# Kernel tuning notes

Hardware: AMD Instinct MI355X
Metric: run time of the kernel (lower is better)

The kernel has to match this reference:

```python
import jax, jax.numpy as jnp
import numpy as np

B, S, D = 1, 2048, 2048
HQ, HKV = 32, 8
HD = D // HQ            # 64
G = HQ // HKV           # 4 query heads per kv head


def setup_inputs() -> dict:
    key = jax.random.key(0)
    ks = jax.random.split(key, 5)
    x = jax.random.normal(ks[0], (B, S, D), jnp.float32)
    # RoPE tables (theta = 10000), shape [S, HD//2]
    inv_freq = 1.0 / (10000.0 ** (np.arange(0, HD, 2, dtype=np.float64) / HD))
    angles = np.outer(np.arange(S, dtype=np.float64), inv_freq)
    freqs_cos = jnp.asarray(np.cos(angles), jnp.float32)
    freqs_sin = jnp.asarray(np.sin(angles), jnp.float32)
    # additive causal mask [1,1,S,S]: 0 on/below diagonal, large negative above
    i = jnp.arange(S)
    causal_mask = jnp.where(i[None, :] <= i[:, None], 0.0, -1e9).astype(jnp.float32)[None, None]
    sc = 1.0 / np.sqrt(D)
    Wq = jax.random.normal(ks[1], (D, HQ * HD), jnp.float32) * sc
    Wk = jax.random.normal(ks[2], (D, HKV * HD), jnp.float32) * sc
    Wv = jax.random.normal(ks[3], (D, HKV * HD), jnp.float32) * sc
    Wo = jax.random.normal(ks[4], (D, D), jnp.float32) * sc
    return {"x": x, "freqs_cos": freqs_cos, "freqs_sin": freqs_sin,
            "causal_mask": causal_mask, "Wq": Wq, "Wk": Wk, "Wv": Wv, "Wo": Wo}


def _rope(t, cos, sin):
    # t: [B,S,H,HD]; complex multiply on interleaved (even, odd) pairs
    b, s, h, d = t.shape
    t2 = t.reshape(b, s, h, d // 2, 2)
    t0, t1 = t2[..., 0], t2[..., 1]
    c = cos[None, :, None, :]
    sn = sin[None, :, None, :]
    out = jnp.stack([t0 * c - t1 * sn, t0 * sn + t1 * c], axis=-1)
    return out.reshape(b, s, h, d)


def reference(x, freqs_cos, freqs_sin, causal_mask, Wq, Wk, Wv, Wo):
    b, s, _ = x.shape
    q = (x @ Wq).reshape(b, s, HQ, HD)
    k = (x @ Wk).reshape(b, s, HKV, HD)
    v = (x @ Wv).reshape(b, s, HKV, HD)
    q = _rope(q, freqs_cos, freqs_sin)
    k = _rope(k, freqs_cos, freqs_sin)
    # GQA without materializing repeat_kv: group query heads per kv head
    q = q.transpose(0, 2, 1, 3).reshape(b, HKV, G, s, HD)   # [b,kv,g,s,d]
    k = k.transpose(0, 2, 1, 3)                              # [b,kv,s,d]
    v = v.transpose(0, 2, 1, 3)                              # [b,kv,s,d]
    scores = jnp.einsum('bkgsd,bktd->bkgst', q, k) / jnp.sqrt(jnp.float32(HD))
    scores = scores + causal_mask[:, :, None]                # [1,1,1,S,S] broadcast
    probs = jax.nn.softmax(scores, axis=-1)
    out = jnp.einsum('bkgst,bktd->bkgsd', probs, v)          # [b,kv,g,s,d]
    out = out.transpose(0, 3, 1, 2, 4).reshape(b, s, D)      # merge heads in (kv,g) order
    return out @ Wo
```

## Files before the change

### kernel.cpp

```cpp
#include <hip/hip_runtime.h>

#define SEQ 2048
#define DMODEL 2048

typedef __attribute__((ext_vector_type(8))) _Float16 half8;
typedef __attribute__((ext_vector_type(4))) float f32x4;
typedef __attribute__((ext_vector_type(16))) float f32x16;

typedef const __attribute__((address_space(1))) void* gptr_t;
typedef __attribute__((address_space(3))) void* lptr_t;

static __device__ __forceinline__ void gload16(const void* g, void* l) {
  __builtin_amdgcn_global_load_lds((gptr_t)g, (lptr_t)l, 16, 0, 0);
}

static __device__ __forceinline__ unsigned short f2h(float f) {
  _Float16 h = (_Float16)f;
  union { _Float16 h; unsigned short u; } v; v.h = h;
  return v.u;
}

static __device__ __forceinline__ unsigned int pkh2(float a, float b) {
  union { __fp16 __attribute__((ext_vector_type(2))) h; unsigned int u; } v;
  v.h = __builtin_amdgcn_cvt_pkrtz(a, b);
  return v.u;
}

__global__ void k_cvt(const float* __restrict__ in, unsigned short* __restrict__ out, int n) {
  int i = (blockIdx.x * 256 + threadIdx.x) * 4;
  if (i >= n) return;
  float4 v = *(const float4*)(in + i);
  ushort4 o;
  o.x = f2h(v.x); o.y = f2h(v.y); o.z = f2h(v.z); o.w = f2h(v.w);
  *(ushort4*)(out + i) = o;
}

__global__ void k_tcvt(const float* __restrict__ in, unsigned short* __restrict__ out,
                       int K, int N, int ldin) {
  __shared__ float tile[32][33];
  int n0 = blockIdx.x * 32, k0 = blockIdx.y * 32;
  int tx = threadIdx.x, ty = threadIdx.y;
  #pragma unroll
  for (int j = ty; j < 32; j += 8)
    tile[j][tx] = in[(long)(k0 + j) * ldin + n0 + tx];
  __syncthreads();
  #pragma unroll
  for (int j = ty; j < 32; j += 8)
    out[(long)(n0 + j) * K + k0 + tx] = f2h(tile[tx][j]);
}

__global__ void k_tvp(const unsigned short* __restrict__ in, unsigned short* __restrict__ out) {
  __shared__ unsigned short tile[32][33];
  int c0 = blockIdx.x * 32, s0 = blockIdx.y * 32;
  int tx = threadIdx.x, ty = threadIdx.y;
  #pragma unroll
  for (int j = ty; j < 32; j += 8)
    tile[j][tx] = in[(long)(s0 + j) * 512 + c0 + tx];
  __syncthreads();
  #pragma unroll
  for (int j = ty; j < 32; j += 8) {
    int c = c0 + j;
    int s = s0 + tx;
    int sp = (s & ~12) | ((s & 8) >> 1) | ((s & 4) << 1);
    out[((long)(c >> 6) * 64 + (c & 63)) * SEQ + sp] = tile[tx][j];
  }
}

static __device__ __forceinline__ bool gemm_core(const unsigned short* __restrict__ A,
                                                 const unsigned short* __restrict__ B,
                                                 int K, char* SM, long m0, long n0,
                                                 int& wmO, int& wnO, f32x4 acc[4][4]) {
  int t = threadIdx.x;
  int l = t & 63, w = t >> 6;
  int ks = w & 1, wm = (w >> 2) & 1, wn = (w >> 1) & 1;
  int lr = l & 15, lh = l >> 4;
  wmO = wm; wnO = wn;
  unsigned short* As = (unsigned short*)SM;
  unsigned short* Bs = (unsigned short*)(SM + 32768);

  const unsigned short* Ag = A + (m0 + (t >> 3)) * K + (((t & 7) ^ ((t >> 3) & 7)) * 8);
  const unsigned short* Bg = B + (n0 + (t >> 3)) * K + (((t & 7) ^ ((t >> 3) & 7)) * 8);

  #pragma unroll
  for (int i = 0; i < 4; i++)
    #pragma unroll
    for (int j = 0; j < 4; j++)
      acc[i][j] = (f32x4){0.f, 0.f, 0.f, 0.f};

#define STG(buf, k0) do { \
    gload16(Ag + (k0), As + (buf) * 8192 + t * 8); \
    gload16(Ag + 64 * K + (k0), As + (buf) * 8192 + 4096 + t * 8); \
    gload16(Bg + (k0), Bs + (buf) * 8192 + t * 8); \
    gload16(Bg + 64 * K + (k0), Bs + (buf) * 8192 + 4096 + t * 8); \
  } while (0)

  int T = K >> 6;
  STG(0, 0);
  asm volatile("s_waitcnt vmcnt(0)" ::: "memory");
  __builtin_amdgcn_s_barrier();

  for (int ph = 0; ph < T; ph++) {
    if (ph + 1 < T) STG((ph + 1) & 1, (ph + 1) * 64);
    const unsigned short* Ab = As + (ph & 1) * 8192;
    const unsigned short* Bb = Bs + (ph & 1) * 8192;
    half8 a[4], b[4];
    #pragma unroll
    for (int mf = 0; mf < 4; mf++) {
      int ra = wm * 64 + mf * 16 + lr;
      a[mf] = *(const half8*)&Ab[ra * 64 + (((ks * 4 + lh) ^ (ra & 7)) * 8)];
    }
    #pragma unroll
    for (int nf = 0; nf < 4; nf++) {
      int rb = wn * 64 + nf * 16 + lr;
      b[nf] = *(const half8*)&Bb[rb * 64 + (((ks * 4 + lh) ^ (rb & 7)) * 8)];
    }
    #pragma unroll
    for (int mf = 0; mf < 4; mf++)
      #pragma unroll
      for (int nf = 0; nf < 4; nf++)
        acc[mf][nf] = __builtin_amdgcn_mfma_f32_16x16x32_f16(a[mf], b[nf], acc[mf][nf], 0, 0, 0);
    asm volatile("s_waitcnt vmcnt(0)" ::: "memory");
    __builtin_amdgcn_s_barrier();
  }
#undef STG

  __syncthreads();
  float* red = (float*)SM;
  int p = wm * 2 + wn;
  if (ks == 1) {
    #pragma unroll
    for (int mf = 0; mf < 4; mf++)
      #pragma unroll
      for (int nf = 0; nf < 4; nf++)
        *(f32x4*)&red[p * 4096 + l * 64 + (((mf * 4 + nf) ^ (l & 15)) << 2)] = acc[mf][nf];
  }
  __syncthreads();
  if (ks == 0) {
    #pragma unroll
    for (int mf = 0; mf < 4; mf++)
      #pragma unroll
      for (int nf = 0; nf < 4; nf++)
        acc[mf][nf] += *(const f32x4*)&red[p * 4096 + l * 64 + (((mf * 4 + nf) ^ (l & 15)) << 2)];
  }
  return ks == 0;
}

__global__ __launch_bounds__(512) void k_gemm(const unsigned short* __restrict__ A,
                                              const unsigned short* __restrict__ B,
                                              float* __restrict__ C, int M, int N, int K) {
  __shared__ __align__(16) char SM[65536];
  int l = threadIdx.x & 63;
  int lr = l & 15, lh = l >> 4;
  long m0 = (long)blockIdx.y * 128, n0 = (long)blockIdx.x * 128;
  f32x4 acc[4][4];
  int wm, wn;
  bool own = gemm_core(A, B, K, SM, m0, n0, wm, wn, acc);
  if (own) {
    #pragma unroll
    for (int mf = 0; mf < 4; mf++)
      #pragma unroll
      for (int nf = 0; nf < 4; nf++)
        #pragma unroll
        for (int i = 0; i < 4; i++)
          C[(m0 + wm * 64 + mf * 16 + lh * 4 + i) * N + n0 + wn * 64 + nf * 16 + lr] = acc[mf][nf][i];
  }
}

__global__ __launch_bounds__(512) void k_gemm_qkv(const unsigned short* __restrict__ A,
                                                  const unsigned short* __restrict__ B,
                                                  unsigned short* __restrict__ Qr,
                                                  unsigned short* __restrict__ Kr,
                                                  unsigned short* __restrict__ Vr,
                                                  const float* __restrict__ fc,
                                                  const float* __restrict__ fs, int K) {
  __shared__ __align__(16) char SM[65536];
  int l = threadIdx.x & 63;
  int lr = l & 15, lh = l >> 4;
  long m0 = (long)blockIdx.y * 128, n0 = (long)blockIdx.x * 128;
  f32x4 acc[4][4];
  int wm, wn;
  bool own = gemm_core(A, B, K, SM, m0, n0, wm, wn, acc);
  if (!own) return;

  const float SC = 0.125f * 1.44269504f;
  int n0i = (int)n0;
  if (n0i < 2560) {
    bool isQ = n0i < 2048;
    float scl = isQ ? SC : 1.0f;
    #pragma unroll
    for (int mf = 0; mf < 4; mf++)
      #pragma unroll
      for (int i = 0; i < 4; i++) {
        int row = (int)m0 + wm * 64 + mf * 16 + lh * 4 + i;
        const float* fcr = fc + row * 32;
        const float* fsr = fs + row * 32;
        #pragma unroll
        for (int nf = 0; nf < 4; nf++) {
          float v = acc[mf][nf][i];
          float pv = __shfl_xor(v, 1);
          int col = n0i + wn * 64 + nf * 16 + lr;
          int j = (col & 63) >> 1;
          float c_ = fcr[j] * scl, s_ = fsr[j] * scl;
          float o = (lr & 1) ? (pv * s_ + v * c_) : (v * c_ - pv * s_);
          if (isQ) Qr[(long)row * 2048 + col] = f2h(o);
          else {
            int cc = col - 2048;
            Kr[((long)(cc >> 6) * SEQ + row) * 64 + (cc & 63)] = f2h(o);
          }
        }
      }
  } else {
    #pragma unroll
    for (int mf = 0; mf < 4; mf++)
      #pragma unroll
      for (int i = 0; i < 4; i++) {
        int row = (int)m0 + wm * 64 + mf * 16 + lh * 4 + i;
        #pragma unroll
        for (int nf = 0; nf < 4; nf++) {
          int col = n0i + wn * 64 + nf * 16 + lr;
          Vr[(long)row * 512 + (col - 2560)] = f2h(acc[mf][nf][i]);
        }
      }
  }
}

template <bool DG>
static __device__ __forceinline__ void attn_tile(const unsigned short* __restrict__ Ks,
                                                 const unsigned short* __restrict__ Vs,
                                                 int q, int hs, const half8 (&Qf)[4],
                                                 f32x16& O0, f32x16& O1, float& lsum) {
  half8 Kf[4], Vf[2][2];
  #pragma unroll
  for (int d = 0; d < 4; d++) {
    int e0 = d * 16 + 8 * hs;
    Kf[d] = *(const half8*)&Ks[q * 64 + (e0 ^ ((q & 7) << 3))];
  }
  #pragma unroll
  for (int ks = 0; ks < 2; ks++)
    #pragma unroll
    for (int nf = 0; nf < 2; nf++)
      Vf[ks][nf] = *(const half8*)&Vs[(2 * ks + hs) * 512 + (q + 32 * nf) * 8];

  f32x16 S;
  #pragma unroll
  for (int r = 0; r < 16; r++) S[r] = 0.f;
  #pragma unroll
  for (int d = 0; d < 4; d++)
    S = __builtin_amdgcn_mfma_f32_32x32x16_f16(Kf[d], Qf[d], S, 0, 0, 0);

  float p[16];
  #pragma unroll
  for (int r = 0; r < 16; r++) {
    float v = S[r];
    if (DG) {
      int key = (r & 3) + 8 * (r >> 2) + 4 * hs;
      if (key > q) v = -1e30f;
    }
    p[r] = __builtin_exp2f(v - 8.0f);
    lsum += p[r];
  }

  union { unsigned int u[4]; half8 hh; } f0, f1;
  #pragma unroll
  for (int c = 0; c < 4; c++) {
    f0.u[c] = pkh2(p[2 * c], p[2 * c + 1]);
    f1.u[c] = pkh2(p[8 + 2 * c], p[9 + 2 * c]);
  }

  O0 = __builtin_amdgcn_mfma_f32_32x32x16_f16(f0.hh, Vf[0][0], O0, 0, 0, 0);
  O0 = __builtin_amdgcn_mfma_f32_32x32x16_f16(f1.hh, Vf[1][0], O0, 0, 0, 0);
  O1 = __builtin_amdgcn_mfma_f32_32x32x16_f16(f0.hh, Vf[0][1], O1, 0, 0, 0);
  O1 = __builtin_amdgcn_mfma_f32_32x32x16_f16(f1.hh, Vf[1][1], O1, 0, 0, 0);
}

__global__ __launch_bounds__(256) void k_attn(const unsigned short* __restrict__ Qr,
                                              const unsigned short* __restrict__ Kr,
                                              const unsigned short* __restrict__ Vg,
                                              unsigned short* __restrict__ AO) {
  __shared__ unsigned short KT[2][8192];
  __shared__ unsigned short VT[2][8192];
  __shared__ float gbuf[4][32];

  int tt = threadIdx.x;
  int wid = tt >> 6, l = tt & 63;
  int q = l & 31, hs = l >> 5;
  int h = blockIdx.x, hkv = h >> 2;
  int by = (int)gridDim.y - 1 - blockIdx.y;
  int dt = 4 * by + wid;
  int q0 = by * 128 + wid * 32;

  const unsigned short* Kh = Kr + (long)hkv * SEQ * 64;
  const unsigned short* Vh = Vg + (long)hkv * 64 * SEQ;

  int skr = tt >> 3, skc = tt & 7;
  const unsigned short* Ksrc = Kh + (long)skr * 64 + ((skc * 8) ^ ((skr & 7) << 3));
  const unsigned short* Vsrc = Vh + (long)(tt & 63) * SEQ + ((tt >> 6) * 8);

#define ASTAGE(si) do { \
    int buf_ = (si) & 1; \
    _Pragma("unroll") for (int sub_ = 0; sub_ < 4; sub_++) { \
      int t0_ = ((si) * 4 + sub_) * 32; \
      gload16(Ksrc + (long)t0_ * 64, &KT[buf_][sub_ * 2048 + tt * 8]); \
      gload16(Vsrc + t0_, &VT[buf_][sub_ * 2048 + tt * 8]); \
    } \
  } while (0)

  half8 Qf[4];
  #pragma unroll
  for (int d = 0; d < 4; d++)
    Qf[d] = *(const half8*)&Qr[(long)(q0 + q) * 2048 + h * 64 + d * 16 + 8 * hs];

  f32x16 O0, O1;
  #pragma unroll
  for (int r = 0; r < 16; r++) { O0[r] = 0.f; O1[r] = 0.f; }
  float lsum = 0.f;

  ASTAGE(0);
  asm volatile("s_waitcnt vmcnt(0)" ::: "memory");
  __builtin_amdgcn_s_barrier();

  for (int si = 0; si <= by; si++) {
    if (si + 1 <= by) ASTAGE(si + 1);

    int buf = si & 1;
    const unsigned short* Kb = &KT[buf][0];
    const unsigned short* Vb = &VT[buf][0];
    int rem = dt - si * 4 + 1;
    if (rem > 4) {
      attn_tile<false>(Kb, Vb, q, hs, Qf, O0, O1, lsum);
      attn_tile<false>(Kb + 2048, Vb + 2048, q, hs, Qf, O0, O1, lsum);
      attn_tile<false>(Kb + 4096, Vb + 4096, q, hs, Qf, O0, O1, lsum);
      attn_tile<false>(Kb + 6144, Vb + 6144, q, hs, Qf, O0, O1, lsum);
    } else if (rem > 0) {
      for (int sub = 0; sub < rem - 1; sub++)
        attn_tile<false>(Kb + sub * 2048, Vb + sub * 2048, q, hs, Qf, O0, O1, lsum);
      attn_tile<true>(Kb + (rem - 1) * 2048, Vb + (rem - 1) * 2048, q, hs, Qf, O0, O1, lsum);
    }

    asm volatile("s_waitcnt vmcnt(0)" ::: "memory");
    __builtin_amdgcn_s_barrier();
  }
#undef ASTAGE

  lsum += __shfl_xor(lsum, 32);
  if (l < 32) gbuf[wid][l] = 1.f / lsum;
  asm volatile("" ::: "memory");
  #pragma unroll
  for (int r = 0; r < 16; r++) {
    int row = (r & 3) + 8 * (r >> 2) + 4 * hs;
    float ri = gbuf[wid][row];
    AO[(long)(q0 + row) * 2048 + h * 64 + q] = f2h(O0[r] * ri);
    AO[(long)(q0 + row) * 2048 + h * 64 + q + 32] = f2h(O1[r] * ri);
  }
}

extern "C" void kernel_launch(void* const* d_in, const int* in_sizes, int n_in,
                              void* d_out, int out_size, void* d_ws, size_t ws_size,
                              hipStream_t stream) {
  const float* x  = (const float*)d_in[0];
  const float* fc = (const float*)d_in[1];
  const float* fs = (const float*)d_in[2];
  const float* Wq = (const float*)d_in[4];
  const float* Wk = (const float*)d_in[5];
  const float* Wv = (const float*)d_in[6];
  const float* Wo = (const float*)d_in[7];
  float* out = (float*)d_out;

  char* ws = (char*)d_ws;
  unsigned short* xb  = (unsigned short*)(ws);
  unsigned short* WT  = (unsigned short*)(ws + (8l  << 20));
  unsigned short* WoT = (unsigned short*)(ws + (20l << 20));
  unsigned short* Qr  = (unsigned short*)(ws + (28l << 20));
  unsigned short* Kr  = (unsigned short*)(ws + (36l << 20));
  unsigned short* Vr  = (unsigned short*)(ws + (38l << 20));
  unsigned short* Vt  = (unsigned short*)(ws + (40l << 20));
  unsigned short* AO  = xb;

  dim3 tb(32, 8);
  k_cvt<<<4096, 256, 0, stream>>>(x, xb, 2048 * 2048);
  k_tcvt<<<dim3(64, 64), tb, 0, stream>>>(Wq, WT, 2048, 2048, 2048);
  k_tcvt<<<dim3(16, 64), tb, 0, stream>>>(Wk, WT + 2048l * 2048, 2048, 512, 512);
  k_tcvt<<<dim3(16, 64), tb, 0, stream>>>(Wv, WT + 2560l * 2048, 2048, 512, 512);
  k_tcvt<<<dim3(64, 64), tb, 0, stream>>>(Wo, WoT, 2048, 2048, 2048);

  k_gemm_qkv<<<dim3(24, 16), 512, 0, stream>>>(xb, WT, Qr, Kr, Vr, fc, fs, 2048);

  k_tvp<<<dim3(16, 64), tb, 0, stream>>>(Vr, Vt);

  k_attn<<<dim3(32, 16), 256, 0, stream>>>(Qr, Kr, Vt, AO);

  k_gemm<<<dim3(16, 16), 512, 0, stream>>>(AO, WoT, out, 2048, 2048, 2048);
}
```

Before: 155.7 us.

## Split attention KV range across two blocks and merge partial sums

Each query block's causal KV range is split into two halves handled by separate blocks (a split-KV scheme), doubling the attention grid from 512 to 1024 blocks to improve load balance and CU occupancy. Unnormalized fp16 partial outputs and row sums go to workspace, and a new merge kernel adds them and normalizes. The per-tile row-sum accumulation is also spread over four independent accumulators to shorten the dependency chain. In exchange it adds an extra kernel launch plus writing and reading two 2048x2048 fp16 partial buffers, and the unnormalized fp16 partial outputs could lose precision.

Result: faster. 151.7 us (-2.6%).

```diff
diff --git a/kernel.cpp b/kernel.cpp
--- a/kernel.cpp
+++ b/kernel.cpp
@@ -228,7 +228,7 @@
 static __device__ __forceinline__ void attn_tile(const unsigned short* __restrict__ Ks,
                                                  const unsigned short* __restrict__ Vs,
                                                  int q, int hs, const half8 (&Qf)[4],
-                                                 f32x16& O0, f32x16& O1, float& lsum) {
+                                                 f32x16& O0, f32x16& O1, f32x4& lsum4) {
   half8 Kf[4], Vf[2][2];
   #pragma unroll
   for (int d = 0; d < 4; d++) {
@@ -257,7 +257,7 @@
       if (key > q) v = -1e30f;
     }
     p[r] = __builtin_exp2f(v - 8.0f);
-    lsum += p[r];
+    lsum4[r & 3] += p[r];
   }
 
   union { unsigned int u[4]; half8 hh; } f0, f1;
@@ -276,16 +276,19 @@
 __global__ __launch_bounds__(256) void k_attn(const unsigned short* __restrict__ Qr,
                                               const unsigned short* __restrict__ Kr,
                                               const unsigned short* __restrict__ Vg,
-                                              unsigned short* __restrict__ AO) {
+                                              unsigned short* __restrict__ Op,
+                                              float* __restrict__ Lp) {
   __shared__ unsigned short KT[2][8192];
   __shared__ unsigned short VT[2][8192];
-  __shared__ float gbuf[4][32];
 
   int tt = threadIdx.x;
   int wid = tt >> 6, l = tt & 63;
   int q = l & 31, hs = l >> 5;
   int h = blockIdx.x, hkv = h >> 2;
-  int by = (int)gridDim.y - 1 - blockIdx.y;
+  int y = blockIdx.y;
+  int by = 15 - (y >> 1), z = y & 1;
+  int h8 = (by + 2) >> 1;
+  int sb = z ? h8 : 0, se = z ? by + 1 : h8;
   int dt = 4 * by + wid;
   int q0 = by * 128 + wid * 32;
 
@@ -313,45 +316,61 @@
   f32x16 O0, O1;
   #pragma unroll
   for (int r = 0; r < 16; r++) { O0[r] = 0.f; O1[r] = 0.f; }
-  float lsum = 0.f;
-
-  ASTAGE(0);
-  asm volatile("s_waitcnt vmcnt(0)" ::: "memory");
-  __builtin_amdgcn_s_barrier();
-
-  for (int si = 0; si <= by; si++) {
-    if (si + 1 <= by) ASTAGE(si + 1);
-
-    int buf = si & 1;
-    const unsigned short* Kb = &KT[buf][0];
-    const unsigned short* Vb = &VT[buf][0];
-    int rem = dt - si * 4 + 1;
-    if (rem > 4) {
-      attn_tile<false>(Kb, Vb, q, hs, Qf, O0, O1, lsum);
-      attn_tile<false>(Kb + 2048, Vb + 2048, q, hs, Qf, O0, O1, lsum);
-      attn_tile<false>(Kb + 4096, Vb + 4096, q, hs, Qf, O0, O1, lsum);
-      attn_tile<false>(Kb + 6144, Vb + 6144, q, hs, Qf, O0, O1, lsum);
-    } else if (rem > 0) {
-      for (int sub = 0; sub < rem - 1; sub++)
-        attn_tile<false>(Kb + sub * 2048, Vb + sub * 2048, q, hs, Qf, O0, O1, lsum);
-      attn_tile<true>(Kb + (rem - 1) * 2048, Vb + (rem - 1) * 2048, q, hs, Qf, O0, O1, lsum);
-    }
-
+  f32x4 lsum4 = (f32x4){0.f, 0.f, 0.f, 0.f};
+
+  if (sb < se) {
+    ASTAGE(sb);
     asm volatile("s_waitcnt vmcnt(0)" ::: "memory");
     __builtin_amdgcn_s_barrier();
+
+    for (int si = sb; si < se; si++) {
+      if (si + 1 < se) ASTAGE(si + 1);
+
+      int buf = si & 1;
+      const unsigned short* Kb = &KT[buf][0];
+      const unsigned short* Vb = &VT[buf][0];
+      int rem = dt - si * 4 + 1;
+      if (rem > 4) {
+        attn_tile<false>(Kb, Vb, q, hs, Qf, O0, O1, lsum4);
+        attn_tile<false>(Kb + 2048, Vb + 2048, q, hs, Qf, O0, O1, lsum4);
+        attn_tile<false>(Kb + 4096, Vb + 4096, q, hs, Qf, O0, O1, lsum4);
+        attn_tile<false>(Kb + 6144, Vb + 6144, q, hs, Qf, O0, O1, lsum4);
+      } else if (rem > 0) {
+        for (int sub = 0; sub < rem - 1; sub++)
+          attn_tile<false>(Kb + sub * 2048, Vb + sub * 2048, q, hs, Qf, O0, O1, lsum4);
+        attn_tile<true>(Kb + (rem - 1) * 2048, Vb + (rem - 1) * 2048, q, hs, Qf, O0, O1, lsum4);
+      }
+
+      asm volatile("s_waitcnt vmcnt(0)" ::: "memory");
+      __builtin_amdgcn_s_barrier();
+    }
   }
 #undef ASTAGE
 
-  lsum += __shfl_xor(lsum, 32);
-  if (l < 32) gbuf[wid][l] = 1.f / lsum;
-  asm volatile("" ::: "memory");
+  float ls = lsum4[0] + lsum4[1] + lsum4[2] + lsum4[3];
+  ls += __shfl_xor(ls, 32);
+  if (l < 32) Lp[z * 65536 + h * 2048 + q0 + l] = ls;
+  unsigned short* Oz = Op + (long)z * 2048 * 2048;
   #pragma unroll
   for (int r = 0; r < 16; r++) {
     int row = (r & 3) + 8 * (r >> 2) + 4 * hs;
-    float ri = gbuf[wid][row];
-    AO[(long)(q0 + row) * 2048 + h * 64 + q] = f2h(O0[r] * ri);
-    AO[(long)(q0 + row) * 2048 + h * 64 + q + 32] = f2h(O1[r] * ri);
-  }
+    Oz[(long)(q0 + row) * 2048 + h * 64 + q] = f2h(O0[r]);
+    Oz[(long)(q0 + row) * 2048 + h * 64 + q + 32] = f2h(O1[r]);
+  }
+}
+
+__global__ void k_merge(const unsigned short* __restrict__ Op, const float* __restrict__ Lp,
+                        unsigned short* __restrict__ AO) {
+  int row = blockIdx.x, t = threadIdx.x;
+  int col = t * 8, h = col >> 6;
+  float li = 1.f / (Lp[h * 2048 + row] + Lp[65536 + h * 2048 + row]);
+  half8 a = *(const half8*)&Op[(long)row * 2048 + col];
+  half8 b = *(const half8*)&Op[4194304l + (long)row * 2048 + col];
+  half8 o;
+  #pragma unroll
+  for (int j = 0; j < 8; j++)
+    o[j] = (_Float16)(((float)a[j] + (float)b[j]) * li);
+  *(half8*)&AO[(long)row * 2048 + col] = o;
 }
 
 extern "C" void kernel_launch(void* const* d_in, const int* in_sizes, int n_in,
@@ -374,6 +393,8 @@
   unsigned short* Kr  = (unsigned short*)(ws + (36l << 20));
   unsigned short* Vr  = (unsigned short*)(ws + (38l << 20));
   unsigned short* Vt  = (unsigned short*)(ws + (40l << 20));
+  unsigned short* Opp = (unsigned short*)(ws + (44l << 20));
+  float*          Lp  = (float*)(ws + (60l << 20));
   unsigned short* AO  = xb;
 
   dim3 tb(32, 8);
@@ -387,7 +408,8 @@
 
   k_tvp<<<dim3(16, 64), tb, 0, stream>>>(Vr, Vt);
 
-  k_attn<<<dim3(32, 16), 256, 0, stream>>>(Qr, Kr, Vt, AO);
+  k_attn<<<dim3(32, 32), 256, 0, stream>>>(Qr, Kr, Vt, Opp, Lp);
+  k_merge<<<2048, 256, 0, stream>>>(Opp, Lp, AO);
 
   k_gemm<<<dim3(16, 16), 512, 0, stream>>>(AO, WoT, out, 2048, 2048, 2048);
 }
```
